# Kernel tuning notes

Measured on AMD Instinct MI355X. Metric: run time of the kernel, lower is better.

Reference implementation:

```python
import jax, jax.numpy as jnp
import numpy as np

N_NODES = 100000
N_EDGES = 1600000
NFEAT = 128
NHID = 64  # layer widths: NFEAT -> 2*NHID -> NHID


def gcn_conv(x, edge_index, edge_weight, W, b):
    """PyG GCNConv: add self-loops, symmetric D^-1/2 (A+I) D^-1/2 normalization."""
    n = x.shape[0]
    h = x @ W  # [N, out]
    src = edge_index[0]
    dst = edge_index[1]
    # degree at destination including self-loop weight 1
    deg = jax.ops.segment_sum(edge_weight, dst, num_segments=n) + 1.0
    dinv = jax.lax.rsqrt(deg)  # deg >= 1, always finite
    norm = dinv[src] * edge_weight * dinv[dst]  # [E]
    agg = jax.ops.segment_sum(h[src] * norm[:, None], dst, num_segments=n)
    agg = agg + h * (dinv * dinv)[:, None]  # self-loop contribution: 1/deg
    return agg + b


def setup_inputs() -> dict:
    key = jax.random.key(0)
    k1, k2, k3, k4, k5, k6 = jax.random.split(key, 6)
    x = jax.random.normal(k1, (N_NODES, NFEAT), dtype=jnp.float32)
    edge_index = jax.random.randint(k2, (2, N_EDGES), 0, N_NODES, dtype=jnp.int64)
    edge_weight = jnp.ones((N_EDGES,), dtype=jnp.float32)
    # GCNConv weights (glorot-ish scale)
    W1 = jax.random.normal(k3, (NFEAT, 2 * NHID), dtype=jnp.float32) / np.sqrt(NFEAT)
    b1 = jnp.zeros((2 * NHID,), dtype=jnp.float32)
    W2 = jax.random.normal(k4, (2 * NHID, NHID), dtype=jnp.float32) / np.sqrt(2 * NHID)
    b2 = jnp.zeros((NHID,), dtype=jnp.float32)
    return {"x": x, "edge_index": edge_index, "edge_weight": edge_weight,
            "W1": W1, "b1": b1, "W2": W2, "b2": b2}


def reference(x, edge_index, edge_weight, W1, b1, W2, b2):
    # GCN_body forward, eval mode (dropout = identity, use_ln/layer_norm_first = False)
    h = jax.nn.relu(gcn_conv(x, edge_index, edge_weight, W1, b1))
    h = jax.nn.relu(gcn_conv(h, edge_index, edge_weight, W2, b2))
    return h
```

## Files before the change

### kernel.cpp

```cpp
#include <hip/hip_runtime.h>

static constexpr int NN = 100000;
static constexpr int NE = 1600000;
static constexpr int BK = 391;
static constexpr int BK2 = 392;
static constexpr int BCAP = 4864;
static constexpr int NBA = 512;
static constexpr int PCAP = 32;
static constexpr int CHUNK = NE / NBA;

typedef _Float16 f16x8 __attribute__((ext_vector_type(8)));
typedef float f32x4 __attribute__((ext_vector_type(4)));

__global__ __launch_bounds__(512) void binA_kernel(const int* __restrict__ src,
                                                   const int* __restrict__ dst,
                                                   const float* __restrict__ w,
                                                   int* __restrict__ cnts,
                                                   long long* __restrict__ binned) {
  __shared__ int hist[BK2];
  __shared__ int localoff[BK2];
  __shared__ int wsum[4];
  __shared__ unsigned long long ebuf[CHUNK];
  __shared__ unsigned int dinfo[CHUNK];
  __shared__ unsigned short bkts[CHUNK];
  const int t = threadIdx.x;
  const int blk = blockIdx.x;
  const int e0 = blk * CHUNK;
  const int e1 = e0 + CHUNK;

  for (int i = t; i < BK2; i += 512) hist[i] = 0;
  __syncthreads();
  for (int e = e0 + t; e < e1; e += 512) {
    int d = dst[e];
    int bkt = d >> 8;
    dinfo[e - e0] = ((unsigned)bkt << 8) | (unsigned)(d & 255);
    atomicAdd(&hist[bkt], 1);
  }
  __syncthreads();
  for (int i = t; i < BK; i += 512) cnts[i * NBA + blk] = min(hist[i], PCAP);

  int h0 = 0, h1 = 0, c = 0;
  if (t < 196) {
    h0 = hist[2 * t];
    h1 = hist[2 * t + 1];
    c = h0 + h1;
  }
  if (t < 256) {
    const int lane = t & 63;
    int incl = c;
#pragma unroll
    for (int d2 = 1; d2 < 64; d2 <<= 1) {
      int v2 = __shfl_up(incl, d2, 64);
      if (lane >= d2) incl += v2;
    }
    if (lane == 63) wsum[t >> 6] = incl;
    __syncthreads();
    int wbase = 0;
#pragma unroll
    for (int ww = 0; ww < 4; ++ww) wbase += (ww < (t >> 6)) ? wsum[ww] : 0;
    if (t < 196) {
      int ex = wbase + incl - c;
      localoff[2 * t] = ex;
      localoff[2 * t + 1] = ex + h0;
    }
  } else {
    __syncthreads();
  }
  __syncthreads();
  for (int i = t; i < BK2; i += 512) hist[i] = 0;
  __syncthreads();

  for (int e = e0 + t; e < e1; e += 512) {
    unsigned di = dinfo[e - e0];
    int bkt = (int)(di >> 8);
    int slot = atomicAdd(&hist[bkt], 1);
    int pos = localoff[bkt] + slot;
    unsigned lo = (unsigned)src[e] | ((di & 255u) << 20);
    ebuf[pos] = ((unsigned long long)__float_as_uint(w[e]) << 32) | lo;
    bkts[pos] = (unsigned short)bkt;
  }
  __syncthreads();

  for (int pos = t; pos < CHUNK; pos += 512) {
    int bkt = bkts[pos];
    int slot = pos - localoff[bkt];
    if (slot < PCAP)
      binned[((size_t)bkt * NBA + blk) * PCAP + slot] = (long long)ebuf[pos];
  }
}

__global__ __launch_bounds__(256) void buildB_kernel(const int* __restrict__ cnts,
                                                     long long* __restrict__ binned,
                                                     int2* __restrict__ meta,
                                                     float* __restrict__ dinv) {
  __shared__ long long eb[BCAP];
  __shared__ int scnt[NBA];
  __shared__ int segbase[NBA];
  __shared__ int cnt[256];
  __shared__ int off[256];
  __shared__ int cur[256];
  __shared__ float degs[256];
  __shared__ int wsum[4];
  __shared__ int tot_s;
  const int b = blockIdx.x;
  const int t = threadIdx.x;
  long long* gb = binned + (size_t)b * NBA * PCAP;

  scnt[t] = cnts[b * NBA + t];
  scnt[t + 256] = cnts[b * NBA + t + 256];
  __syncthreads();

  {
    int s0 = scnt[2 * t];
    int s1 = scnt[2 * t + 1];
    int c2 = s0 + s1;
    const int lane = t & 63;
    int incl = c2;
#pragma unroll
    for (int d2 = 1; d2 < 64; d2 <<= 1) {
      int v2 = __shfl_up(incl, d2, 64);
      if (lane >= d2) incl += v2;
    }
    if (lane == 63) wsum[t >> 6] = incl;
    __syncthreads();
    int wbase = 0;
#pragma unroll
    for (int ww = 0; ww < 4; ++ww) wbase += (ww < (t >> 6)) ? wsum[ww] : 0;
    int ex = wbase + incl - c2;
    segbase[2 * t] = ex;
    segbase[2 * t + 1] = ex + s0;
    if (t == 255) tot_s = ex + c2;
  }
  __syncthreads();
  const int m = min(tot_s, BCAP);

  {
    const int wv = t >> 6;
    const int lane = t & 63;
    for (int g = wv; g < NBA / 8; g += 4) {
      int s = g * 8 + (lane >> 3);
      for (int i = lane & 7; i < scnt[s]; i += 8) {
        int db = segbase[s] + i;
        if (db < BCAP) eb[db] = gb[(size_t)s * PCAP + i];
      }
    }
  }
  cnt[t] = 0;
  degs[t] = 0.f;
  __syncthreads();

  for (int i = t; i < m; i += 256) {
    unsigned long long v = (unsigned long long)eb[i];
    int dl = (int)((v >> 20) & 255u);
    atomicAdd(&cnt[dl], 1);
    atomicAdd(&degs[dl], __uint_as_float((unsigned)(v >> 32)));
  }
  __syncthreads();

  const int lane = t & 63;
  const int c = cnt[t];
  int incl = c;
#pragma unroll
  for (int d2 = 1; d2 < 64; d2 <<= 1) {
    int v2 = __shfl_up(incl, d2, 64);
    if (lane >= d2) incl += v2;
  }
  if (lane == 63) wsum[t >> 6] = incl;
  __syncthreads();
  int wbase = 0;
#pragma unroll
  for (int ww = 0; ww < 4; ++ww) wbase += (ww < (t >> 6)) ? wsum[ww] : 0;
  const int myoff = wbase + incl - c;
  off[t] = myoff;
  cur[t] = 0;
  __syncthreads();

  for (int i = t; i < m; i += 256) {
    long long v = eb[i];
    int dl = (int)(((unsigned long long)v >> 20) & 255u);
    int slot = atomicAdd(&cur[dl], 1);
    gb[off[dl] + slot] = v;
  }

  const int n = b * 256 + t;
  if (n < NN) {
    meta[n] = make_int2(b * NBA * PCAP + myoff, c);
    dinv[n] = rsqrtf(degs[t] + 1.0f);
  }
}

__global__ void wfrag_kernel(const float* __restrict__ W1, const float* __restrict__ W2,
                             _Float16* __restrict__ wf1, _Float16* __restrict__ wf2) {
  int i = blockIdx.x * blockDim.x + threadIdx.x;
  const float* W;
  _Float16* wf;
  int N, idx;
  if (i < 128 * 128) {
    W = W1; wf = wf1; N = 128; idx = i;
  } else if (i < 128 * 128 + 64 * 128) {
    W = W2; wf = wf2; N = 64; idx = i - 128 * 128;
  } else return;
  int j = idx & 7;
  int l = (idx >> 3) & 63;
  int ks = (idx >> 9) & 3;
  int t = idx >> 11;
  int n = t * 16 + (l & 15);
  int k = ks * 32 + (l >> 4) * 8 + j;
  wf[idx] = (_Float16)W[k * N + n];
}

template <int N, typename AT>
__global__ __launch_bounds__(256) void mfma_gemm_kernel(const AT* __restrict__ X,
                                                        const _Float16* __restrict__ wf,
                                                        _Float16* __restrict__ H) {
  constexpr int NT = N / 16;
  const int w = threadIdx.x >> 6;
  const int l = threadIdx.x & 63;
  const int row0 = (blockIdx.x * 4 + w) * 16;
  const int arow = row0 + (l & 15);
  const int kb = (l >> 4) * 8;

  f16x8 a[4];
  if (arow < NN) {
    const AT* xp = X + (size_t)arow * 128 + kb;
#pragma unroll
    for (int ks = 0; ks < 4; ++ks) {
      if constexpr (sizeof(AT) == 4) {
        float4 lo = *(const float4*)(xp + ks * 32);
        float4 hi = *(const float4*)(xp + ks * 32 + 4);
        f16x8 v;
        v[0] = (_Float16)lo.x; v[1] = (_Float16)lo.y;
        v[2] = (_Float16)lo.z; v[3] = (_Float16)lo.w;
        v[4] = (_Float16)hi.x; v[5] = (_Float16)hi.y;
        v[6] = (_Float16)hi.z; v[7] = (_Float16)hi.w;
        a[ks] = v;
      } else {
        a[ks] = *(const f16x8*)(xp + ks * 32);
      }
    }
  } else {
    f16x8 z;
#pragma unroll
    for (int j = 0; j < 8; ++j) z[j] = (_Float16)0.f;
#pragma unroll
    for (int ks = 0; ks < 4; ++ks) a[ks] = z;
  }

  f32x4 acc[NT];
#pragma unroll
  for (int t = 0; t < NT; ++t) acc[t] = {0.f, 0.f, 0.f, 0.f};

  const _Float16* wp = wf + l * 8;
#pragma unroll
  for (int t = 0; t < NT; ++t) {
#pragma unroll
    for (int ks = 0; ks < 4; ++ks) {
      f16x8 b = *(const f16x8*)(wp + (size_t)(t * 4 + ks) * 512);
      acc[t] = __builtin_amdgcn_mfma_f32_16x16x32_f16(a[ks], b, acc[t], 0, 0, 0);
    }
  }

  const int r0 = row0 + (l >> 4) * 4;
  const int c0 = l & 15;
#pragma unroll
  for (int t = 0; t < NT; ++t) {
#pragma unroll
    for (int r = 0; r < 4; ++r) {
      int row = r0 + r;
      if (row < NN) H[(size_t)row * N + t * 16 + c0] = (_Float16)acc[t][r];
    }
  }
}

__global__ __launch_bounds__(256) void gather_gemm_kernel(
    const int2* __restrict__ meta, const long long* __restrict__ csr,
    const _Float16* __restrict__ H, const float* __restrict__ dinv,
    const float* __restrict__ b, const _Float16* __restrict__ wf2,
    _Float16* __restrict__ h2) {
  constexpr int LDA = 136;
  __shared__ _Float16 als[16 * LDA];
  const int t = threadIdx.x;
  const int nl = t >> 4;
  const int node = blockIdx.x * 16 + nl;
  const int g = t & 15;
  const int f = g * 8;

  const int2 mt = meta[node];
  const int lo = mt.x;
  const int hi = mt.x + mt.y;
  const float di = dinv[node];
  const float sl = di * di;

  f16x8 hs = *(const f16x8*)(H + (size_t)node * 128 + f);
  float c[8], aA[8], aB[8];
#pragma unroll
  for (int j = 0; j < 8; ++j) {
    c[j] = fmaf((float)hs[j], sl, b[f + j]);
    aA[j] = 0.f;
    aB[j] = 0.f;
  }

  int i = lo;
  for (; i + 1 < hi; i += 2) {
    unsigned long long v0 = (unsigned long long)csr[i];
    unsigned long long v1 = (unsigned long long)csr[i + 1];
    int s0 = (int)(v0 & 0x1FFFFu);
    int s1 = (int)(v1 & 0x1FFFFu);
    float n0 = dinv[s0] * __uint_as_float((unsigned)(v0 >> 32));
    float n1 = dinv[s1] * __uint_as_float((unsigned)(v1 >> 32));
    f16x8 h0 = *(const f16x8*)(H + (size_t)s0 * 128 + f);
    f16x8 h1 = *(const f16x8*)(H + (size_t)s1 * 128 + f);
#pragma unroll
    for (int j = 0; j < 8; ++j) {
      aA[j] = fmaf((float)h0[j], n0, aA[j]);
      aB[j] = fmaf((float)h1[j], n1, aB[j]);
    }
  }
  if (i < hi) {
    unsigned long long v0 = (unsigned long long)csr[i];
    int s0 = (int)(v0 & 0x1FFFFu);
    float n0 = dinv[s0] * __uint_as_float((unsigned)(v0 >> 32));
    f16x8 h0 = *(const f16x8*)(H + (size_t)s0 * 128 + f);
#pragma unroll
    for (int j = 0; j < 8; ++j) aA[j] = fmaf((float)h0[j], n0, aA[j]);
  }

  f16x8 av;
#pragma unroll
  for (int j = 0; j < 8; ++j)
    av[j] = (_Float16)fmaxf(fmaf(aA[j] + aB[j], di, c[j]), 0.f);
  *(f16x8*)(als + nl * LDA + f) = av;
  __syncthreads();

  const int w = t >> 6;
  const int l = t & 63;
  f32x4 acc = {0.f, 0.f, 0.f, 0.f};
  const _Float16* ap = als + (l & 15) * LDA + (l >> 4) * 8;
  const _Float16* wp = wf2 + (size_t)w * 4 * 512 + l * 8;
#pragma unroll
  for (int ks = 0; ks < 4; ++ks) {
    f16x8 afrag = *(const f16x8*)(ap + ks * 32);
    f16x8 bfrag = *(const f16x8*)(wp + ks * 512);
    acc = __builtin_amdgcn_mfma_f32_16x16x32_f16(afrag, bfrag, acc, 0, 0, 0);
  }
  const int orow = blockIdx.x * 16 + (l >> 4) * 4;
  const int ocol = w * 16 + (l & 15);
#pragma unroll
  for (int r = 0; r < 4; ++r)
    h2[(size_t)(orow + r) * 64 + ocol] = (_Float16)acc[r];
}

__global__ __launch_bounds__(256) void gather64_kernel(
    const int2* __restrict__ meta, const long long* __restrict__ csr,
    const _Float16* __restrict__ H, const float* __restrict__ dinv,
    const float* __restrict__ b, float* __restrict__ out) {
  const int t = threadIdx.x;
  const int node = blockIdx.x * 32 + (t >> 3);
  const int f = (t & 7) * 8;

  const int2 mt = meta[node];
  const int lo = mt.x;
  const int hi = mt.x + mt.y;
  const float di = dinv[node];
  const float sl = di * di;

  f16x8 hs = *(const f16x8*)(H + (size_t)node * 64 + f);
  float c[8], aA[8], aB[8];
#pragma unroll
  for (int j = 0; j < 8; ++j) {
    c[j] = fmaf((float)hs[j], sl, b[f + j]);
    aA[j] = 0.f;
    aB[j] = 0.f;
  }

  int i = lo;
  for (; i + 1 < hi; i += 2) {
    unsigned long long v0 = (unsigned long long)csr[i];
    unsigned long long v1 = (unsigned long long)csr[i + 1];
    int s0 = (int)(v0 & 0x1FFFFu);
    int s1 = (int)(v1 & 0x1FFFFu);
    float n0 = dinv[s0] * __uint_as_float((unsigned)(v0 >> 32));
    float n1 = dinv[s1] * __uint_as_float((unsigned)(v1 >> 32));
    f16x8 h0 = *(const f16x8*)(H + (size_t)s0 * 64 + f);
    f16x8 h1 = *(const f16x8*)(H + (size_t)s1 * 64 + f);
#pragma unroll
    for (int j = 0; j < 8; ++j) {
      aA[j] = fmaf((float)h0[j], n0, aA[j]);
      aB[j] = fmaf((float)h1[j], n1, aB[j]);
    }
  }
  if (i < hi) {
    unsigned long long v0 = (unsigned long long)csr[i];
    int s0 = (int)(v0 & 0x1FFFFu);
    float n0 = dinv[s0] * __uint_as_float((unsigned)(v0 >> 32));
    f16x8 h0 = *(const f16x8*)(H + (size_t)s0 * 64 + f);
#pragma unroll
    for (int j = 0; j < 8; ++j) aA[j] = fmaf((float)h0[j], n0, aA[j]);
  }

  float4 v0, v1;
  v0.x = fmaxf(fmaf(aA[0] + aB[0], di, c[0]), 0.f);
  v0.y = fmaxf(fmaf(aA[1] + aB[1], di, c[1]), 0.f);
  v0.z = fmaxf(fmaf(aA[2] + aB[2], di, c[2]), 0.f);
  v0.w = fmaxf(fmaf(aA[3] + aB[3], di, c[3]), 0.f);
  v1.x = fmaxf(fmaf(aA[4] + aB[4], di, c[4]), 0.f);
  v1.y = fmaxf(fmaf(aA[5] + aB[5], di, c[5]), 0.f);
  v1.z = fmaxf(fmaf(aA[6] + aB[6], di, c[6]), 0.f);
  v1.w = fmaxf(fmaf(aA[7] + aB[7], di, c[7]), 0.f);
  *(float4*)(out + (size_t)node * 64 + f) = v0;
  *(float4*)(out + (size_t)node * 64 + f + 4) = v1;
}

extern "C" void kernel_launch(void* const* d_in, const int* in_sizes, int n_in,
                              void* d_out, int out_size, void* d_ws, size_t ws_size,
                              hipStream_t stream) {
  const float* x  = (const float*)d_in[0];
  const int*   ei = (const int*)d_in[1];
  const float* ew = (const float*)d_in[2];
  const float* W1 = (const float*)d_in[3];
  const float* b1 = (const float*)d_in[4];
  const float* W2 = (const float*)d_in[5];
  const float* b2 = (const float*)d_in[6];
  float* out = (float*)d_out;

  const int* src = ei;
  const int* dst = ei + NE;

  float* wsf        = (float*)d_ws;
  int*   cnts       = (int*)wsf;
  float* dinv       = wsf + BK * NBA;
  int2*  meta       = (int2*)(dinv + NN);
  long long* binned = (long long*)(meta + NN);
  float* fbase      = (float*)(binned + (size_t)BK * NBA * PCAP);
  _Float16* h1      = (_Float16*)fbase;
  _Float16* h2      = (_Float16*)(fbase + (size_t)NN * 64);
  _Float16* wf1     = (_Float16*)(fbase + (size_t)NN * 96);
  _Float16* wf2     = wf1 + 16384;

  binA_kernel<<<NBA, 512, 0, stream>>>(src, dst, ew, cnts, binned);
  buildB_kernel<<<BK, 256, 0, stream>>>(cnts, binned, meta, dinv);
  wfrag_kernel<<<96, 256, 0, stream>>>(W1, W2, wf1, wf2);

  mfma_gemm_kernel<128, float><<<(NN + 63) / 64, 256, 0, stream>>>(x, wf1, h1);
  gather_gemm_kernel<<<NN / 16, 256, 0, stream>>>(meta, binned, h1, dinv, b1, wf2, h2);
  gather64_kernel<<<NN / 32, 256, 0, stream>>>(meta, binned, h2, dinv, b2, out);
}
```

Before: 172.9 us.

## Fuse binning, bucket build and weight fragment prep into one cooperative kernel

Replaces the three preprocessing launches (edge binning, per-bucket CSR build with degree/dinv, weight fragment conversion) with one cooperative kernel that uses a grid-wide sync between the binning and build phases. The weight fragment conversion is spread over the binning blocks, and the build phase now runs with 512 threads per block. The intent is to remove launch overhead and the gaps between kernels. The cost is a grid barrier, a shared 48KB LDS union that may limit occupancy, and a requirement that all 512 blocks be co-resident.

```diff
diff --git a/kernel.cpp b/kernel.cpp
--- a/kernel.cpp
+++ b/kernel.cpp
@@ -1,4 +1,7 @@
 #include <hip/hip_runtime.h>
+#include <hip/hip_cooperative_groups.h>
+
+namespace cg = cooperative_groups;
 
 static constexpr int NN = 100000;
 static constexpr int NE = 1600000;
@@ -12,41 +15,57 @@
 typedef _Float16 f16x8 __attribute__((ext_vector_type(8)));
 typedef float f32x4 __attribute__((ext_vector_type(4)));
 
-__global__ __launch_bounds__(512) void binA_kernel(const int* __restrict__ src,
-                                                   const int* __restrict__ dst,
-                                                   const float* __restrict__ w,
-                                                   int* __restrict__ cnts,
-                                                   long long* __restrict__ binned) {
-  __shared__ int hist[BK2];
-  __shared__ int localoff[BK2];
-  __shared__ int wsum[4];
-  __shared__ unsigned long long ebuf[CHUNK];
-  __shared__ unsigned int dinfo[CHUNK];
-  __shared__ unsigned short bkts[CHUNK];
+__global__ __launch_bounds__(512) void prep_kernel(
+    const int* __restrict__ src, const int* __restrict__ dst,
+    const float* __restrict__ w, const float* __restrict__ W1,
+    const float* __restrict__ W2, int* __restrict__ cnts,
+    long long* __restrict__ binned, int2* __restrict__ meta,
+    float* __restrict__ dinv, _Float16* __restrict__ wf1,
+    _Float16* __restrict__ wf2) {
+  __shared__ __align__(16) unsigned char smem[48 * 1024];
   const int t = threadIdx.x;
   const int blk = blockIdx.x;
-  const int e0 = blk * CHUNK;
-  const int e1 = e0 + CHUNK;
-
-  for (int i = t; i < BK2; i += 512) hist[i] = 0;
-  __syncthreads();
-  for (int e = e0 + t; e < e1; e += 512) {
-    int d = dst[e];
-    int bkt = d >> 8;
-    dinfo[e - e0] = ((unsigned)bkt << 8) | (unsigned)(d & 255);
-    atomicAdd(&hist[bkt], 1);
-  }
-  __syncthreads();
-  for (int i = t; i < BK; i += 512) cnts[i * NBA + blk] = min(hist[i], PCAP);
-
-  int h0 = 0, h1 = 0, c = 0;
-  if (t < 196) {
-    h0 = hist[2 * t];
-    h1 = hist[2 * t + 1];
-    c = h0 + h1;
-  }
-  if (t < 256) {
-    const int lane = t & 63;
+  const int lane = t & 63;
+
+  {
+    int* hist = (int*)smem;
+    int* localoff = (int*)(smem + 1568);
+    int* wsum = (int*)(smem + 3136);
+    unsigned long long* ebuf = (unsigned long long*)(smem + 3168);
+    unsigned* dinfo = (unsigned*)(smem + 28168);
+    unsigned short* bkts = (unsigned short*)(smem + 40668);
+
+    {
+      int idx = blk * 48 + t;
+      if (t < 48) {
+        const float* W; _Float16* wf; int N, id2;
+        if (idx < 16384) { W = W1; wf = wf1; N = 128; id2 = idx; }
+        else             { W = W2; wf = wf2; N = 64;  id2 = idx - 16384; }
+        int j = id2 & 7, l = (id2 >> 3) & 63, ks = (id2 >> 9) & 3, tt = id2 >> 11;
+        int n = tt * 16 + (l & 15);
+        int k = ks * 32 + (l >> 4) * 8 + j;
+        wf[id2] = (_Float16)W[k * N + n];
+      }
+    }
+
+    const int e0 = blk * CHUNK;
+    for (int i = t; i < BK2; i += 512) hist[i] = 0;
+    __syncthreads();
+    for (int e = t; e < CHUNK; e += 512) {
+      int d = dst[e0 + e];
+      int bkt = d >> 8;
+      dinfo[e] = ((unsigned)bkt << 8) | (unsigned)(d & 255);
+      atomicAdd(&hist[bkt], 1);
+    }
+    __syncthreads();
+    for (int i = t; i < BK; i += 512) cnts[i * NBA + blk] = min(hist[i], PCAP);
+
+    int h0 = 0, h1v = 0, c = 0;
+    if (t < 196) {
+      h0 = hist[2 * t];
+      h1v = hist[2 * t + 1];
+      c = h0 + h1v;
+    }
     int incl = c;
 #pragma unroll
     for (int d2 = 1; d2 < 64; d2 <<= 1) {
@@ -57,156 +76,128 @@
     __syncthreads();
     int wbase = 0;
 #pragma unroll
-    for (int ww = 0; ww < 4; ++ww) wbase += (ww < (t >> 6)) ? wsum[ww] : 0;
+    for (int ww = 0; ww < 8; ++ww) wbase += (ww < (t >> 6)) ? wsum[ww] : 0;
     if (t < 196) {
       int ex = wbase + incl - c;
       localoff[2 * t] = ex;
       localoff[2 * t + 1] = ex + h0;
     }
-  } else {
-    __syncthreads();
-  }
-  __syncthreads();
-  for (int i = t; i < BK2; i += 512) hist[i] = 0;
-  __syncthreads();
-
-  for (int e = e0 + t; e < e1; e += 512) {
-    unsigned di = dinfo[e - e0];
-    int bkt = (int)(di >> 8);
-    int slot = atomicAdd(&hist[bkt], 1);
-    int pos = localoff[bkt] + slot;
-    unsigned lo = (unsigned)src[e] | ((di & 255u) << 20);
-    ebuf[pos] = ((unsigned long long)__float_as_uint(w[e]) << 32) | lo;
-    bkts[pos] = (unsigned short)bkt;
-  }
-  __syncthreads();
-
-  for (int pos = t; pos < CHUNK; pos += 512) {
-    int bkt = bkts[pos];
-    int slot = pos - localoff[bkt];
-    if (slot < PCAP)
-      binned[((size_t)bkt * NBA + blk) * PCAP + slot] = (long long)ebuf[pos];
-  }
-}
-
-__global__ __launch_bounds__(256) void buildB_kernel(const int* __restrict__ cnts,
-                                                     long long* __restrict__ binned,
-                                                     int2* __restrict__ meta,
-                                                     float* __restrict__ dinv) {
-  __shared__ long long eb[BCAP];
-  __shared__ int scnt[NBA];
-  __shared__ int segbase[NBA];
-  __shared__ int cnt[256];
-  __shared__ int off[256];
-  __shared__ int cur[256];
-  __shared__ float degs[256];
-  __shared__ int wsum[4];
-  __shared__ int tot_s;
-  const int b = blockIdx.x;
-  const int t = threadIdx.x;
-  long long* gb = binned + (size_t)b * NBA * PCAP;
-
-  scnt[t] = cnts[b * NBA + t];
-  scnt[t + 256] = cnts[b * NBA + t + 256];
-  __syncthreads();
-
-  {
-    int s0 = scnt[2 * t];
-    int s1 = scnt[2 * t + 1];
-    int c2 = s0 + s1;
-    const int lane = t & 63;
+    __syncthreads();
+    for (int i = t; i < BK2; i += 512) hist[i] = 0;
+    __syncthreads();
+
+    for (int e = t; e < CHUNK; e += 512) {
+      unsigned di = dinfo[e];
+      int bkt = (int)(di >> 8);
+      int slot = atomicAdd(&hist[bkt], 1);
+      int pos = localoff[bkt] + slot;
+      unsigned lo = (unsigned)src[e0 + e] | ((di & 255u) << 20);
+      ebuf[pos] = ((unsigned long long)__float_as_uint(w[e0 + e]) << 32) | lo;
+      bkts[pos] = (unsigned short)bkt;
+    }
+    __syncthreads();
+
+    for (int pos = t; pos < CHUNK; pos += 512) {
+      int bkt = bkts[pos];
+      int slot = pos - localoff[bkt];
+      if (slot < PCAP)
+        binned[((size_t)bkt * NBA + blk) * PCAP + slot] = (long long)ebuf[pos];
+    }
+  }
+
+  __threadfence();
+  cg::this_grid().sync();
+
+  if (blk < BK) {
+    long long* eb = (long long*)smem;
+    int* scnt = (int*)(smem + 38912);
+    int* segbase = (int*)(smem + 40960);
+    int* cnt = (int*)(smem + 43008);
+    int* off = (int*)(smem + 44032);
+    int* cur = (int*)(smem + 45056);
+    float* degs = (float*)(smem + 46080);
+    int* wsum2 = (int*)(smem + 47104);
+    int* totp = (int*)(smem + 47136);
+    const int b = blk;
+    long long* gb = binned + (size_t)b * NBA * PCAP;
+
+    int c2 = cnts[b * NBA + t];
+    scnt[t] = c2;
     int incl = c2;
 #pragma unroll
     for (int d2 = 1; d2 < 64; d2 <<= 1) {
       int v2 = __shfl_up(incl, d2, 64);
       if (lane >= d2) incl += v2;
     }
-    if (lane == 63) wsum[t >> 6] = incl;
+    if (lane == 63) wsum2[t >> 6] = incl;
     __syncthreads();
     int wbase = 0;
 #pragma unroll
-    for (int ww = 0; ww < 4; ++ww) wbase += (ww < (t >> 6)) ? wsum[ww] : 0;
+    for (int ww = 0; ww < 8; ++ww) wbase += (ww < (t >> 6)) ? wsum2[ww] : 0;
     int ex = wbase + incl - c2;
-    segbase[2 * t] = ex;
-    segbase[2 * t + 1] = ex + s0;
-    if (t == 255) tot_s = ex + c2;
-  }
-  __syncthreads();
-  const int m = min(tot_s, BCAP);
-
-  {
-    const int wv = t >> 6;
-    const int lane = t & 63;
-    for (int g = wv; g < NBA / 8; g += 4) {
-      int s = g * 8 + (lane >> 3);
-      for (int i = lane & 7; i < scnt[s]; i += 8) {
-        int db = segbase[s] + i;
+    segbase[t] = ex;
+    if (t == 511) *totp = ex + c2;
+    __syncthreads();
+    const int m = min(*totp, BCAP);
+
+#pragma unroll
+    for (int pass = 0; pass < 8; ++pass) {
+      int s = pass * 64 + (t >> 3);
+      int sc = scnt[s];
+      int sb = segbase[s];
+      for (int i = t & 7; i < sc; i += 8) {
+        int db = sb + i;
         if (db < BCAP) eb[db] = gb[(size_t)s * PCAP + i];
       }
     }
-  }
-  cnt[t] = 0;
-  degs[t] = 0.f;
-  __syncthreads();
-
-  for (int i = t; i < m; i += 256) {
-    unsigned long long v = (unsigned long long)eb[i];
-    int dl = (int)((v >> 20) & 255u);
-    atomicAdd(&cnt[dl], 1);
-    atomicAdd(&degs[dl], __uint_as_float((unsigned)(v >> 32)));
-  }
-  __syncthreads();
-
-  const int lane = t & 63;
-  const int c = cnt[t];
-  int incl = c;
-#pragma unroll
-  for (int d2 = 1; d2 < 64; d2 <<= 1) {
-    int v2 = __shfl_up(incl, d2, 64);
-    if (lane >= d2) incl += v2;
-  }
-  if (lane == 63) wsum[t >> 6] = incl;
-  __syncthreads();
-  int wbase = 0;
-#pragma unroll
-  for (int ww = 0; ww < 4; ++ww) wbase += (ww < (t >> 6)) ? wsum[ww] : 0;
-  const int myoff = wbase + incl - c;
-  off[t] = myoff;
-  cur[t] = 0;
-  __syncthreads();
-
-  for (int i = t; i < m; i += 256) {
-    long long v = eb[i];
-    int dl = (int)(((unsigned long long)v >> 20) & 255u);
-    int slot = atomicAdd(&cur[dl], 1);
-    gb[off[dl] + slot] = v;
-  }
-
-  const int n = b * 256 + t;
-  if (n < NN) {
-    meta[n] = make_int2(b * NBA * PCAP + myoff, c);
-    dinv[n] = rsqrtf(degs[t] + 1.0f);
-  }
-}
-
-__global__ void wfrag_kernel(const float* __restrict__ W1, const float* __restrict__ W2,
-                             _Float16* __restrict__ wf1, _Float16* __restrict__ wf2) {
-  int i = blockIdx.x * blockDim.x + threadIdx.x;
-  const float* W;
-  _Float16* wf;
-  int N, idx;
-  if (i < 128 * 128) {
-    W = W1; wf = wf1; N = 128; idx = i;
-  } else if (i < 128 * 128 + 64 * 128) {
-    W = W2; wf = wf2; N = 64; idx = i - 128 * 128;
-  } else return;
-  int j = idx & 7;
-  int l = (idx >> 3) & 63;
-  int ks = (idx >> 9) & 3;
-  int t = idx >> 11;
-  int n = t * 16 + (l & 15);
-  int k = ks * 32 + (l >> 4) * 8 + j;
-  wf[idx] = (_Float16)W[k * N + n];
+    if (t < 256) {
+      cnt[t] = 0;
+      degs[t] = 0.f;
+    }
+    __syncthreads();
+
+    for (int i = t; i < m; i += 512) {
+      unsigned long long v = (unsigned long long)eb[i];
+      int dl = (int)((v >> 20) & 255u);
+      atomicAdd(&cnt[dl], 1);
+      atomicAdd(&degs[dl], __uint_as_float((unsigned)(v >> 32)));
+    }
+    __syncthreads();
+
+    int cc = (t < 256) ? cnt[t] : 0;
+    int incl2 = cc;
+#pragma unroll
+    for (int d2 = 1; d2 < 64; d2 <<= 1) {
+      int v2 = __shfl_up(incl2, d2, 64);
+      if (lane >= d2) incl2 += v2;
+    }
+    if (lane == 63) wsum2[t >> 6] = incl2;
+    __syncthreads();
+    int wb2 = 0;
+#pragma unroll
+    for (int ww = 0; ww < 4; ++ww) wb2 += (ww < (t >> 6)) ? wsum2[ww] : 0;
+    const int myoff = wb2 + incl2 - cc;
+    if (t < 256) {
+      off[t] = myoff;
+      cur[t] = 0;
+    }
+    __syncthreads();
+
+    for (int i = t; i < m; i += 512) {
+      long long v = eb[i];
+      int dl = (int)(((unsigned long long)v >> 20) & 255u);
+      int slot = atomicAdd(&cur[dl], 1);
+      gb[off[dl] + slot] = v;
+    }
+
+    if (t < 256) {
+      int n = b * 256 + t;
+      if (n < NN) {
+        meta[n] = make_int2(b * NBA * PCAP + myoff, cc);
+        dinv[n] = rsqrtf(degs[t] + 1.0f);
+      }
+    }
+  }
 }
 
 template <int N, typename AT>
@@ -437,9 +428,11 @@
   _Float16* wf1     = (_Float16*)(fbase + (size_t)NN * 96);
   _Float16* wf2     = wf1 + 16384;
 
-  binA_kernel<<<NBA, 512, 0, stream>>>(src, dst, ew, cnts, binned);
-  buildB_kernel<<<BK, 256, 0, stream>>>(cnts, binned, meta, dinv);
-  wfrag_kernel<<<96, 256, 0, stream>>>(W1, W2, wf1, wf2);
+  void* args[] = {(void*)&src, (void*)&dst, (void*)&ew, (void*)&W1, (void*)&W2,
+                  (void*)&cnts, (void*)&binned, (void*)&meta, (void*)&dinv,
+                  (void*)&wf1, (void*)&wf2};
+  hipLaunchCooperativeKernel((const void*)prep_kernel, dim3(NBA), dim3(512),
+                             args, 0, stream);
 
   mfma_gemm_kernel<128, float><<<(NN + 63) / 64, 256, 0, stream>>>(x, wf1, h1);
   gather_gemm_kernel<<<NN / 16, 256, 0, stream>>>(meta, binned, h1, dinv, b1, wf2, h2);
```

Result: slower. 320.7 us (+85.5%).
